# Performance work log

Measured on AMD Instinct MI355X. Metric: run time of the kernel, lower is better.

Reference implementation:

```python
import math
import jax, jax.numpy as jnp
import numpy as np

HIDDEN = 128
NUM_REL = 48
NUM_BASES = 8
NUM_ENT = 50000
NUM_SPECIAL = 64
NUM_EDGES = 600000


def setup_inputs() -> dict:
    key = jax.random.key(0)
    ks = jax.random.split(key, 8)
    edge_index = jax.random.randint(ks[0], (2, NUM_EDGES), 0, NUM_ENT, dtype=jnp.int64)
    edge_type = jax.random.randint(ks[1], (NUM_EDGES,), 0, NUM_REL, dtype=jnp.int64)
    # node embeddings: uniform(-stdv, stdv), stdv = sqrt(6/(N+d)) as in the torch init
    stdv = math.sqrt(6.0 / (NUM_ENT + HIDDEN))
    node_embeds = jax.random.uniform(ks[2], (NUM_ENT, HIDDEN), jnp.float32, -stdv, stdv)
    # RGCN basis-decomposition params (PyG RGCNConv): weight [B, d, d], comp [R, B]
    basis = jax.random.normal(ks[3], (NUM_BASES, HIDDEN, HIDDEN), jnp.float32) * (1.0 / math.sqrt(HIDDEN))
    comp = jax.random.normal(ks[4], (NUM_REL, NUM_BASES), jnp.float32) * (1.0 / math.sqrt(NUM_BASES))
    root = jax.random.normal(ks[5], (HIDDEN, HIDDEN), jnp.float32) * (1.0 / math.sqrt(HIDDEN))
    bias = jnp.zeros((HIDDEN,), jnp.float32)
    special_emb = jax.random.normal(ks[6], (NUM_SPECIAL, HIDDEN), jnp.float32) * 0.02
    special_emb = special_emb.at[0].set(0.0)  # padding_idx=0
    return {"edge_index": edge_index, "edge_type": edge_type,
            "node_embeds": node_embeds, "basis": basis, "comp": comp,
            "root": root, "bias": bias, "special_emb": special_emb}


def rgcn_conv(x, edge_index, edge_type, basis, comp, root, bias):
    # PyG RGCNConv with basis decomposition, aggr='mean', root weight + bias.
    # W_r = sum_b comp[r, b] * basis[b]; out[n] = x[n] @ root + bias
    #        + sum_r mean_{e: type(e)=r, dst(e)=n} (x[src(e)] @ W_r)
    N = x.shape[0]
    R, B = comp.shape
    src, dst = edge_index[0], edge_index[1]
    # per-(relation, dst) in-degree for the per-relation mean aggregation
    seg = edge_type * N + dst  # [E]
    cnt = jax.ops.segment_sum(jnp.ones(src.shape[0], x.dtype), seg, num_segments=R * N)
    norm = 1.0 / jnp.maximum(cnt[seg], 1.0)  # [E]
    w = comp[edge_type] * norm[:, None]  # [E, B] per-edge basis coefficients / count
    x_src = x[src]  # [E, d] gather (dominant memory traffic)
    out = x @ root + bias  # [N, d]
    # linearity: mean over edges of (x_src @ W) == (weighted-sum of x_src) @ basis_b per basis
    for b in range(B):
        agg = jax.ops.segment_sum(x_src * w[:, b:b + 1], dst, num_segments=N)  # [N, d]
        out = out + agg @ basis[b]
    return out


def reference(edge_index, edge_type, node_embeds, basis, comp, root, bias, special_emb):
    node_out = rgcn_conv(node_embeds, edge_index, edge_type, basis, comp, root, bias)
    return jnp.concatenate([node_out, special_emb], axis=0)  # [N + S, d]
```

## Files before the change

kernel.cpp:

```cpp
#include <hip/hip_runtime.h>

#define NDIM 128
#define NBASES 8
#define KDIM 1152
#define GTILE 16
#define APITCH 1160

typedef __attribute__((ext_vector_type(8))) __bf16 bfrag;
typedef __attribute__((ext_vector_type(4))) float f32x4;

__device__ __forceinline__ float bf2f(unsigned short b) {
    return __uint_as_float(((unsigned)b) << 16);
}
__device__ __forceinline__ unsigned short f2bf(float f) {
    unsigned u = __float_as_uint(f);
    unsigned r = u + 0x7FFFu + ((u >> 16) & 1u);
    return (unsigned short)(r >> 16);
}
__device__ __forceinline__ unsigned pack2bf(float lo, float hi) {
    return (unsigned)f2bf(lo) | ((unsigned)f2bf(hi) << 16);
}
__device__ __forceinline__ float loadF(const void* p, int idx, int isf32) {
    return isf32 ? ((const float*)p)[idx] : bf2f(((const unsigned short*)p)[idx]);
}

__global__ void detect_k(const unsigned short* __restrict__ xs,
                         const int* __restrict__ ei, int* __restrict__ meta) {
    if (threadIdx.x != 0 || blockIdx.x != 0) return;
    const uint4* xv = (const uint4*)xs;
    unsigned f32m = 0;
    uint4 bx[16];
    #pragma unroll
    for (int i = 0; i < 16; ++i) bx[i] = xv[i];
    #pragma unroll
    for (int i = 0; i < 16; ++i) {
        unsigned a = bx[i].x, b = bx[i].y, c = bx[i].z, d = bx[i].w;
        f32m |= (((a & 0xFFFFu) >> 7) & 0xFFu) > 124u;
        f32m |= (((b & 0xFFFFu) >> 7) & 0xFFu) > 124u;
        f32m |= (((c & 0xFFFFu) >> 7) & 0xFFu) > 124u;
        f32m |= (((d & 0xFFFFu) >> 7) & 0xFFu) > 124u;
    }
    const uint4* ev = (const uint4*)ei;
    unsigned nzm = 0;
    for (int r = 0; r < 4; ++r) {
        uint4 be[16];
        #pragma unroll
        for (int i = 0; i < 16; ++i) be[i] = ev[r * 16 + i];
        #pragma unroll
        for (int i = 0; i < 16; ++i) nzm |= be[i].y | be[i].w;
    }
    meta[0] = f32m ? 1 : 0;
    meta[1] = nzm ? 0 : 1;
}

__global__ void misc_k(const void* __restrict__ basis, const void* __restrict__ root,
                       const void* __restrict__ se, const int* __restrict__ meta,
                       unsigned short* __restrict__ BT, void* __restrict__ out,
                       int scount, int sbase) {
    int t = blockIdx.x * 256 + threadIdx.x;
    int isf32 = meta[0];
    if (t < NDIM * KDIM) {
        int j = t / KDIM, k = t % KDIM;
        float v = (k < NBASES * NDIM) ? loadF(basis, k * NDIM + j, isf32)
                                      : loadF(root, (k - NBASES * NDIM) * NDIM + j, isf32);
        BT[t] = f2bf(v);
    } else {
        int u = t - NDIM * KDIM;
        if (u < scount) {
            float v = loadF(se, u, isf32);
            if (isf32) ((float*)out)[sbase + u] = v;
            else       ((unsigned short*)out)[sbase + u] = f2bf(v);
        }
    }
}

__global__ void hist_k(const int* __restrict__ ei, int E, int N,
                       const int* __restrict__ meta, int* __restrict__ hist) {
    int e = blockIdx.x * 256 + threadIdx.x;
    if (e >= E) return;
    int dst = meta[1] ? ei[2 * (E + e)] : ei[E + e];
    dst = min(max(dst, 0), N - 1);
    atomicAdd(&hist[dst], 1);
}

__global__ void scanA_k(const int* __restrict__ hist, int N,
                        int* __restrict__ offsets, int* __restrict__ bsum) {
    __shared__ int s[1024];
    int tid = threadIdx.x;
    int idx = blockIdx.x * 1024 + tid;
    int v = (idx < N) ? hist[idx] : 0;
    s[tid] = v;
    __syncthreads();
    for (int off = 1; off < 1024; off <<= 1) {
        int t = 0;
        if (tid >= off) t = s[tid - off];
        __syncthreads();
        if (tid >= off) s[tid] += t;
        __syncthreads();
    }
    if (idx < N) offsets[idx] = s[tid] - v;
    if (tid == 1023) bsum[blockIdx.x] = s[1023];
}
__global__ void scanB_k(const int* __restrict__ bsum, int NB, int N,
                        int* __restrict__ bpre, int* __restrict__ offsets) {
    __shared__ int s[64];
    int tid = threadIdx.x;
    int v = (tid < NB) ? bsum[tid] : 0;
    s[tid] = v;
    __syncthreads();
    for (int off = 1; off < 64; off <<= 1) {
        int t = 0;
        if (tid >= off) t = s[tid - off];
        __syncthreads();
        if (tid >= off) s[tid] += t;
        __syncthreads();
    }
    if (tid < NB) bpre[tid] = s[tid] - v;
    if (tid == NB - 1) offsets[N] = s[tid];
}
__global__ void scanC_k(int N, const int* __restrict__ bpre, int* __restrict__ offsets) {
    int idx = blockIdx.x * 1024 + threadIdx.x;
    if (idx < N) offsets[idx] += bpre[blockIdx.x];
}

__global__ void scatter_k(const int* __restrict__ ei, const int* __restrict__ et,
                          int E, int N, const int* __restrict__ meta,
                          const int* __restrict__ offsets, int* __restrict__ cursor,
                          int* __restrict__ sorted) {
    int e = blockIdx.x * 256 + threadIdx.x;
    if (e >= E) return;
    int i64 = meta[1];
    int src = i64 ? ei[2 * e] : ei[e];
    int dst = i64 ? ei[2 * (E + e)] : ei[E + e];
    int rel = i64 ? et[2 * e] : et[e];
    src = min(max(src, 0), N - 1);
    dst = min(max(dst, 0), N - 1);
    rel = rel & 63;
    int pos = offsets[dst] + atomicAdd(&cursor[dst], 1);
    sorted[pos] = src | (rel << 16);
}

__global__ __launch_bounds__(1024) void rgcn_main_k(
    const void* __restrict__ x, const void* __restrict__ comp,
    const void* __restrict__ bias, const unsigned short* __restrict__ BT,
    const int* __restrict__ meta, const int* __restrict__ offsets,
    const int* __restrict__ sorted, void* __restrict__ out, int N)
{
    __shared__ alignas(16) unsigned short A_lds[GTILE * APITCH];
    __shared__ float2 comp_lds[48 * 4];
    const int tid  = threadIdx.x;
    const int lane = tid & 63;
    const int wave = tid >> 6;
    const int isf32 = meta[0];

    for (int t = tid; t < 48 * NBASES; t += 1024)
        ((float*)comp_lds)[t] = loadF(comp, t, isf32);
    __syncthreads();

    const int nodeBase = blockIdx.x * GTILE;
    const int dg = lane & 15;
    const int bs = lane >> 4;

    {
        const int n = nodeBase + wave;
        float acc0[8], acc1[8];
        #pragma unroll
        for (int i = 0; i < 8; ++i) { acc0[i] = 0.f; acc1[i] = 0.f; }

        if (n < N) {
            const int start = offsets[n], end = offsets[n + 1];

            int myCnt = 0;
            for (int c = start; c < end; c += 64) {
                int sv = (c + lane < end) ? sorted[c + lane] : -1;
                int mm = min(64, end - c);
                for (int j = 0; j < mm; ++j) {
                    int rv = __shfl(sv, j) >> 16;
                    myCnt += (rv == lane) ? 1 : 0;
                }
            }
            float myCntF = (float)myCnt;

            if (!isf32) {
                const unsigned short* xh = (const unsigned short*)x;
                for (int c = start; c < end; c += 64) {
                    int sv = (c + lane < end) ? sorted[c + lane] : -1;
                    int mm = min(64, end - c);
                    int j = 0;
                    for (; j + 4 <= mm; j += 4) {
                        unsigned q0 = (unsigned)__shfl(sv, j);
                        unsigned q1 = (unsigned)__shfl(sv, j + 1);
                        unsigned q2 = (unsigned)__shfl(sv, j + 2);
                        unsigned q3 = (unsigned)__shfl(sv, j + 3);
                        uint4 x0 = *(const uint4*)(xh + (size_t)(q0 & 0xFFFFu) * NDIM + dg * 8);
                        uint4 x1 = *(const uint4*)(xh + (size_t)(q1 & 0xFFFFu) * NDIM + dg * 8);
                        uint4 x2 = *(const uint4*)(xh + (size_t)(q2 & 0xFFFFu) * NDIM + dg * 8);
                        uint4 x3 = *(const uint4*)(xh + (size_t)(q3 & 0xFFFFu) * NDIM + dg * 8);
                        #pragma unroll
                        for (int u = 0; u < 4; ++u) {
                            unsigned qq = (u == 0) ? q0 : (u == 1) ? q1 : (u == 2) ? q2 : q3;
                            uint4  xa = (u == 0) ? x0 : (u == 1) ? x1 : (u == 2) ? x2 : x3;
                            int rel = (int)(qq >> 16);
                            float cf = __shfl(myCntF, rel);
                            float norm = 1.0f / fmaxf(cf, 1.0f);
                            float2 cw = comp_lds[rel * 4 + bs];
                            float w0 = cw.x * norm, w1 = cw.y * norm;
                            #pragma unroll
                            for (int i = 0; i < 4; ++i) {
                                float lo = __uint_as_float(xa[i] << 16);
                                float hi = __uint_as_float(xa[i] & 0xFFFF0000u);
                                acc0[2*i]   += w0 * lo;  acc0[2*i+1] += w0 * hi;
                                acc1[2*i]   += w1 * lo;  acc1[2*i+1] += w1 * hi;
                            }
                        }
                    }
                    for (; j < mm; ++j) {
                        unsigned qq = (unsigned)__shfl(sv, j);
                        int rel = (int)(qq >> 16);
                        float cf = __shfl(myCntF, rel);
                        float norm = 1.0f / fmaxf(cf, 1.0f);
                        float2 cw = comp_lds[rel * 4 + bs];
                        float w0 = cw.x * norm, w1 = cw.y * norm;
                        uint4 xa = *(const uint4*)(xh + (size_t)(qq & 0xFFFFu) * NDIM + dg * 8);
                        #pragma unroll
                        for (int i = 0; i < 4; ++i) {
                            float lo = __uint_as_float(xa[i] << 16);
                            float hi = __uint_as_float(xa[i] & 0xFFFF0000u);
                            acc0[2*i]   += w0 * lo;  acc0[2*i+1] += w0 * hi;
                            acc1[2*i]   += w1 * lo;  acc1[2*i+1] += w1 * hi;
                        }
                    }
                }
            } else {
                const float* xf = (const float*)x;
                for (int c = start; c < end; c += 64) {
                    int sv = (c + lane < end) ? sorted[c + lane] : -1;
                    int mm = min(64, end - c);
                    for (int j = 0; j < mm; ++j) {
                        unsigned qq = (unsigned)__shfl(sv, j);
                        int rel = (int)(qq >> 16); int src = (int)(qq & 0xFFFFu);
                        float cf = __shfl(myCntF, rel);
                        float norm = 1.0f / fmaxf(cf, 1.0f);
                        float2 cw = comp_lds[rel * 4 + bs];
                        float w0 = cw.x * norm, w1 = cw.y * norm;
                        #pragma unroll
                        for (int i = 0; i < 8; ++i) {
                            float xv = xf[(size_t)src * NDIM + dg * 8 + i];
                            acc0[i] += w0 * xv; acc1[i] += w1 * xv;
                        }
                    }
                }
            }
        }

        unsigned short* row = &A_lds[wave * APITCH];
        uint4 p0, p1;
        p0.x = pack2bf(acc0[0], acc0[1]); p0.y = pack2bf(acc0[2], acc0[3]);
        p0.z = pack2bf(acc0[4], acc0[5]); p0.w = pack2bf(acc0[6], acc0[7]);
        p1.x = pack2bf(acc1[0], acc1[1]); p1.y = pack2bf(acc1[2], acc1[3]);
        p1.z = pack2bf(acc1[4], acc1[5]); p1.w = pack2bf(acc1[6], acc1[7]);
        *(uint4*)(row + (bs * 2 + 0) * NDIM + dg * 8) = p0;
        *(uint4*)(row + (bs * 2 + 1) * NDIM + dg * 8) = p1;
        if (bs == 0) {
            uint4 xr = {0, 0, 0, 0};
            if (n < N) {
                if (!isf32) {
                    xr = *(const uint4*)((const unsigned short*)x + (size_t)n * NDIM + dg * 8);
                } else {
                    const float* xf = (const float*)x + (size_t)n * NDIM + dg * 8;
                    xr.x = pack2bf(xf[0], xf[1]); xr.y = pack2bf(xf[2], xf[3]);
                    xr.z = pack2bf(xf[4], xf[5]); xr.w = pack2bf(xf[6], xf[7]);
                }
            }
            *(uint4*)(row + NBASES * NDIM + dg * 8) = xr;
        }
    }
    __syncthreads();

    if (wave < 4) {
        const int m = lane & 15;
        const int q = lane >> 4;
        f32x4 C0 = {0,0,0,0}, C1 = {0,0,0,0};
        const unsigned short* arow = &A_lds[m * APITCH];
        const int jb = wave * 32;
        for (int ks = 0; ks < KDIM / 32; ++ks) {
            int k = ks * 32 + q * 8;
            bfrag a  = *(const bfrag*)(arow + k);
            bfrag b0 = *(const bfrag*)(BT + (size_t)(jb +  0 + m) * KDIM + k);
            bfrag b1 = *(const bfrag*)(BT + (size_t)(jb + 16 + m) * KDIM + k);
            C0 = __builtin_amdgcn_mfma_f32_16x16x32_bf16(a, b0, C0, 0, 0, 0);
            C1 = __builtin_amdgcn_mfma_f32_16x16x32_bf16(a, b1, C1, 0, 0, 0);
        }
        #pragma unroll
        for (int t = 0; t < 2; ++t) {
            f32x4 Ct = t ? C1 : C0;
            int j = jb + t * 16 + m;
            float bj = loadF(bias, j, isf32);
            #pragma unroll
            for (int r = 0; r < 4; ++r) {
                int n = nodeBase + q * 4 + r;
                if (n < N) {
                    float v = Ct[r] + bj;
                    if (isf32) ((float*)out)[(size_t)n * NDIM + j] = v;
                    else       ((unsigned short*)out)[(size_t)n * NDIM + j] = f2bf(v);
                }
            }
        }
    }
}

extern "C" void kernel_launch(void* const* d_in, const int* in_sizes, int n_in,
                              void* d_out, int out_size, void* d_ws, size_t ws_size,
                              hipStream_t stream) {
    const int* ei = (const int*)d_in[0];
    const int* et = (const int*)d_in[1];

    const int E = in_sizes[1];
    const int N = in_sizes[2] / NDIM;
    const int S = in_sizes[7] / NDIM;
    const int NB = (N + 1023) / 1024;

    char* ws = (char*)d_ws;
    size_t off = 0;
    int* meta    = (int*)(ws + off); off += 16;
    int* hist    = (int*)(ws + off); off += (size_t)N * 4;
    int* cursor  = (int*)(ws + off); off += (size_t)N * 4;
    int* offsets = (int*)(ws + off); off = (off + (size_t)(N + 1) * 4 + 15) & ~(size_t)15;
    int* bsum    = (int*)(ws + off); off += 64 * 4;
    int* bpre    = (int*)(ws + off); off += 64 * 4;
    unsigned short* BT = (unsigned short*)(ws + off); off += (size_t)NDIM * KDIM * 2;
    int* sorted  = (int*)(ws + off); off += (size_t)E * 4;

    hipMemsetAsync(hist, 0, (size_t)2 * N * 4, stream);

    detect_k<<<1, 64, 0, stream>>>((const unsigned short*)d_in[2], ei, meta);
    misc_k<<<(NDIM * KDIM + S * NDIM + 255) / 256, 256, 0, stream>>>(
        d_in[3], d_in[5], d_in[7], meta, BT, d_out, S * NDIM, N * NDIM);
    hist_k<<<(E + 255) / 256, 256, 0, stream>>>(ei, E, N, meta, hist);
    scanA_k<<<NB, 1024, 0, stream>>>(hist, N, offsets, bsum);
    scanB_k<<<1, 64, 0, stream>>>(bsum, NB, N, bpre, offsets);
    scanC_k<<<NB, 1024, 0, stream>>>(N, bpre, offsets);
    scatter_k<<<(E + 255) / 256, 256, 0, stream>>>(ei, et, E, N, meta, offsets, cursor, sorted);
    rgcn_main_k<<<(N + GTILE - 1) / GTILE, 1024, 0, stream>>>(d_in[2], d_in[4], d_in[6], BT,
                                                              meta, offsets, sorted, d_out, N);
}
```

Before: 341.0 us.

## Fuse preprocessing kernels into one cooperative kernel with grid syncs

```diff
diff --git a/kernel.cpp b/kernel.cpp
--- a/kernel.cpp
+++ b/kernel.cpp
@@ -1,4 +1,7 @@
 #include <hip/hip_runtime.h>
+#include <hip/hip_cooperative_groups.h>
+
+namespace cg = cooperative_groups;
 
 #define NDIM 128
 #define NBASES 8
@@ -22,6 +25,119 @@
 }
 __device__ __forceinline__ float loadF(const void* p, int idx, int isf32) {
     return isf32 ? ((const float*)p)[idx] : bf2f(((const unsigned short*)p)[idx]);
+}
+
+__global__ __launch_bounds__(1024, 8) void prep_k(
+    const unsigned short* xs, const int* ei, const int* et,
+    const void* basis, const void* root, const void* se,
+    int* meta, int* hist, int* cursor, int* offsets, int* bsum, int* bpre,
+    unsigned short* BT, void* out, int* sorted, int E, int N, int S, int sbase)
+{
+    cg::grid_group g = cg::this_grid();
+    __shared__ int s[1024];
+    const int tid = threadIdx.x;
+    const int gt = blockIdx.x * 1024 + tid;
+    const int GT = gridDim.x * 1024;
+    const int NB = (N + 1023) >> 10;
+
+    for (int i = gt; i < 2 * N; i += GT) hist[i] = 0;
+    if (blockIdx.x == 0 && tid == 0) {
+        const uint4* xv = (const uint4*)xs;
+        unsigned f32m = 0;
+        uint4 bx[16];
+        #pragma unroll
+        for (int i = 0; i < 16; ++i) bx[i] = xv[i];
+        #pragma unroll
+        for (int i = 0; i < 16; ++i) {
+            unsigned a = bx[i].x, b = bx[i].y, c = bx[i].z, d = bx[i].w;
+            f32m |= (((a & 0xFFFFu) >> 7) & 0xFFu) > 124u;
+            f32m |= (((b & 0xFFFFu) >> 7) & 0xFFu) > 124u;
+            f32m |= (((c & 0xFFFFu) >> 7) & 0xFFu) > 124u;
+            f32m |= (((d & 0xFFFFu) >> 7) & 0xFFu) > 124u;
+        }
+        const uint4* ev = (const uint4*)ei;
+        unsigned nzm = 0;
+        for (int r = 0; r < 4; ++r) {
+            uint4 be[16];
+            #pragma unroll
+            for (int i = 0; i < 16; ++i) be[i] = ev[r * 16 + i];
+            #pragma unroll
+            for (int i = 0; i < 16; ++i) nzm |= be[i].y | be[i].w;
+        }
+        meta[0] = f32m ? 1 : 0;
+        meta[1] = nzm ? 0 : 1;
+    }
+    g.sync();
+
+    const int isf32 = meta[0], i64 = meta[1];
+
+    const int TOT = NDIM * KDIM + S * NDIM;
+    for (int t = gt; t < TOT; t += GT) {
+        if (t < NDIM * KDIM) {
+            int j = t / KDIM, k = t % KDIM;
+            float v = (k < NBASES * NDIM) ? loadF(basis, k * NDIM + j, isf32)
+                                          : loadF(root, (k - NBASES * NDIM) * NDIM + j, isf32);
+            BT[t] = f2bf(v);
+        } else {
+            int u = t - NDIM * KDIM;
+            float v = loadF(se, u, isf32);
+            if (isf32) ((float*)out)[sbase + u] = v;
+            else       ((unsigned short*)out)[sbase + u] = f2bf(v);
+        }
+    }
+    for (int e = gt; e < E; e += GT) {
+        int dst = i64 ? ei[2 * (E + e)] : ei[E + e];
+        dst = min(max(dst, 0), N - 1);
+        atomicAdd(&hist[dst], 1);
+    }
+    g.sync();
+
+    if (blockIdx.x < NB) {
+        int idx = blockIdx.x * 1024 + tid;
+        int v = (idx < N) ? hist[idx] : 0;
+        s[tid] = v;
+        __syncthreads();
+        for (int off = 1; off < 1024; off <<= 1) {
+            int t2 = 0;
+            if (tid >= off) t2 = s[tid - off];
+            __syncthreads();
+            if (tid >= off) s[tid] += t2;
+            __syncthreads();
+        }
+        if (idx < N) offsets[idx] = s[tid] - v;
+        if (tid == 1023) bsum[blockIdx.x] = s[1023];
+    }
+    g.sync();
+
+    if (blockIdx.x == 0) {
+        int v = (tid < NB) ? bsum[tid] : 0;
+        if (tid < 64) s[tid] = v;
+        __syncthreads();
+        for (int off = 1; off < 64; off <<= 1) {
+            int t2 = 0;
+            if (tid >= off && tid < 64) t2 = s[tid - off];
+            __syncthreads();
+            if (tid >= off && tid < 64) s[tid] += t2;
+            __syncthreads();
+        }
+        if (tid < NB) bpre[tid] = s[tid] - v;
+        if (tid == NB - 1) offsets[N] = s[tid];
+    }
+    g.sync();
+
+    for (int i = gt; i < N; i += GT) offsets[i] += bpre[i >> 10];
+    g.sync();
+
+    for (int e = gt; e < E; e += GT) {
+        int src = i64 ? ei[2 * e] : ei[e];
+        int dst = i64 ? ei[2 * (E + e)] : ei[E + e];
+        int rel = i64 ? et[2 * e] : et[e];
+        src = min(max(src, 0), N - 1);
+        dst = min(max(dst, 0), N - 1);
+        rel = rel & 63;
+        int pos = offsets[dst] + atomicAdd(&cursor[dst], 1);
+        sorted[pos] = src | (rel << 16);
+    }
 }
 
 __global__ void detect_k(const unsigned short* __restrict__ xs,
@@ -245,8 +361,8 @@
                         float w0 = cw.x * norm, w1 = cw.y * norm;
                         #pragma unroll
                         for (int i = 0; i < 8; ++i) {
-                            float xv = xf[(size_t)src * NDIM + dg * 8 + i];
-                            acc0[i] += w0 * xv; acc1[i] += w1 * xv;
+                            float xvv = xf[(size_t)src * NDIM + dg * 8 + i];
+                            acc0[i] += w0 * xvv; acc1[i] += w1 * xvv;
                         }
                     }
                 }
@@ -314,6 +430,7 @@
                               hipStream_t stream) {
     const int* ei = (const int*)d_in[0];
     const int* et = (const int*)d_in[1];
+    const unsigned short* xs = (const unsigned short*)d_in[2];
 
     const int E = in_sizes[1];
     const int N = in_sizes[2] / NDIM;
@@ -331,16 +448,36 @@
     unsigned short* BT = (unsigned short*)(ws + off); off += (size_t)NDIM * KDIM * 2;
     int* sorted  = (int*)(ws + off); off += (size_t)E * 4;
 
-    hipMemsetAsync(hist, 0, (size_t)2 * N * 4, stream);
-
-    detect_k<<<1, 64, 0, stream>>>((const unsigned short*)d_in[2], ei, meta);
-    misc_k<<<(NDIM * KDIM + S * NDIM + 255) / 256, 256, 0, stream>>>(
-        d_in[3], d_in[5], d_in[7], meta, BT, d_out, S * NDIM, N * NDIM);
-    hist_k<<<(E + 255) / 256, 256, 0, stream>>>(ei, E, N, meta, hist);
-    scanA_k<<<NB, 1024, 0, stream>>>(hist, N, offsets, bsum);
-    scanB_k<<<1, 64, 0, stream>>>(bsum, NB, N, bpre, offsets);
-    scanC_k<<<NB, 1024, 0, stream>>>(N, bpre, offsets);
-    scatter_k<<<(E + 255) / 256, 256, 0, stream>>>(ei, et, E, N, meta, offsets, cursor, sorted);
+    int occ = 0;
+    if (hipOccupancyMaxActiveBlocksPerMultiprocessor(&occ, prep_k, 1024, 0) != hipSuccess || occ < 1)
+        occ = 1;
+    int grid = occ * 256;
+    if (grid > 512) grid = 512;
+    if (grid < 64)  grid = 64;
+
+    const void* basis = d_in[3];
+    const void* root  = d_in[5];
+    const void* se    = d_in[7];
+    void* outp = d_out;
+    int sbase = N * NDIM;
+    void* args[] = {(void*)&xs, (void*)&ei, (void*)&et, (void*)&basis, (void*)&root,
+                    (void*)&se, (void*)&meta, (void*)&hist, (void*)&cursor, (void*)&offsets,
+                    (void*)&bsum, (void*)&bpre, (void*)&BT, (void*)&outp, (void*)&sorted,
+                    (void*)&E, (void*)&N, (void*)&S, (void*)&sbase};
+    hipError_t cerr = hipLaunchCooperativeKernel((void*)prep_k, dim3(grid), dim3(1024),
+                                                 args, 0, stream);
+    if (cerr != hipSuccess) {
+        hipMemsetAsync(hist, 0, (size_t)2 * N * 4, stream);
+        detect_k<<<1, 64, 0, stream>>>(xs, ei, meta);
+        misc_k<<<(NDIM * KDIM + S * NDIM + 255) / 256, 256, 0, stream>>>(
+            basis, root, se, meta, BT, d_out, S * NDIM, N * NDIM);
+        hist_k<<<(E + 255) / 256, 256, 0, stream>>>(ei, E, N, meta, hist);
+        scanA_k<<<NB, 1024, 0, stream>>>(hist, N, offsets, bsum);
+        scanB_k<<<1, 64, 0, stream>>>(bsum, NB, N, bpre, offsets);
+        scanC_k<<<NB, 1024, 0, stream>>>(N, bpre, offsets);
+        scatter_k<<<(E + 255) / 256, 256, 0, stream>>>(ei, et, E, N, meta, offsets, cursor, sorted);
+    }
+
     rgcn_main_k<<<(N + GTILE - 1) / GTILE, 1024, 0, stream>>>(d_in[2], d_in[4], d_in[6], BT,
                                                               meta, offsets, sorted, d_out, N);
 }
```

New measurement: 477.0 us. +39.9%, slower.
